# Kernel tuning notes

Hardware: AMD Instinct MI355X
Metric: run time of the kernel (lower is better)

The kernel has to match this reference:

```python
import jax, jax.numpy as jnp
import numpy as np

N = 100000          # query / support points
H = 32              # neighbors per point
CIN = 32
COUT = 64
K = 15              # kernel points
KP_EXTENT = 1.0
KERNEL_RADIUS = KP_EXTENT * 1.5


def setup_inputs() -> dict:
    key = jax.random.key(0)
    k1, k2, k3, k4, k5, k6 = jax.random.split(key, 6)
    query = jax.random.uniform(k1, (N, 3), dtype=jnp.float32)
    support = jax.random.uniform(k2, (N, 3), dtype=jnp.float32)
    edge_indices = jax.random.randint(k3, (N, H), 0, N, dtype=jnp.int32)
    features = jax.random.normal(k4, (N, CIN), dtype=jnp.float32)
    # kernel point positions within kernel radius (fixed, non-trainable)
    K_points = jax.random.normal(k5, (K, 3), dtype=jnp.float32) * (KERNEL_RADIUS / 3.0)
    K_points = K_points.at[0].set(0.0)  # fixed='center'
    # xavier-normal kernel weights [K, CIN, COUT]
    std = jnp.sqrt(2.0 / (CIN + COUT)).astype(jnp.float32)
    K_values = jax.random.normal(k6, (K, CIN, COUT), dtype=jnp.float32) * std
    return {"query": query, "support": support, "edge_indices": edge_indices,
            "features": features, "K_points": K_points, "K_values": K_values}


def reference(query, support, edge_indices, features, K_points, K_values):
    # shadow point / shadow feature for out-of-range indices
    shadow_pt = jnp.ones_like(support[:1]) * 1e6
    support_ext = jnp.concatenate([support, shadow_pt], axis=0)      # [N+1, 3]
    feats_ext = jnp.concatenate([features, jnp.zeros_like(features[:1])], axis=0)  # [N+1, CIN]

    neighbors = support_ext[edge_indices] - query[:, None, :]        # [N, H, 3]
    # squared distances to each kernel point: [N, H, K]
    diff = neighbors[:, :, None, :] - K_points[None, None, :, :]     # [N, H, K, 3]
    sq_distances = jnp.sum(diff * diff, axis=-1)                     # [N, H, K]

    # linear influence, transposed to [N, K, H]
    all_weights = jnp.maximum(1.0 - jnp.sqrt(sq_distances) / KP_EXTENT, 0.0)
    all_weights = jnp.swapaxes(all_weights, 1, 2)                    # [N, K, H]

    # aggregation_mode == 'sum': no masking
    neighborhood_features = feats_ext[edge_indices]                  # [N, H, CIN]
    weighted = jnp.einsum('nkh,nhc->nkc', all_weights, neighborhood_features)  # [N, K, CIN]
    # per-kernel-point matmul then sum over kernel points
    out = jnp.einsum('nkc,kco->no', weighted, K_values)              # [N, COUT]
    return out
```

## Files before the change

### kernel.cpp

```cpp
#include <hip/hip_runtime.h>
#include <hip/hip_bf16.h>

typedef __attribute__((ext_vector_type(8))) short short8;
typedef __attribute__((ext_vector_type(4))) short short4v;
typedef __attribute__((ext_vector_type(4))) float f32x4;
typedef __attribute__((ext_vector_type(4))) int   i32x4;
typedef __attribute__((ext_vector_type(2))) unsigned int u32x2;

#define HH    32
#define CINN  32
#define COUTT 64
#define KNUM  15

__device__ __forceinline__ short bfbits(float f) {
    __hip_bfloat16 h = __float2bfloat16(f);
    short s; __builtin_memcpy(&s, &h, 2); return s;
}

__global__ void cvt_feats_kernel(const float* __restrict__ f,
                                 unsigned short* __restrict__ o, int n4) {
    int i = blockIdx.x * blockDim.x + threadIdx.x;
    if (i < n4) {
        f32x4 v = *(const f32x4*)(f + i * 4);
        short4v s = { bfbits(v.x), bfbits(v.y), bfbits(v.z), bfbits(v.w) };
        *(short4v*)(o + i * 4) = s;
    }
}

__launch_bounds__(256, 4)
__global__ void kpconv_kernel(const float* __restrict__ query,
                              const float* __restrict__ support,
                              const int*   __restrict__ edge,
                              const unsigned short* __restrict__ featsbf,
                              const float* __restrict__ kpts,
                              const float* __restrict__ kvals,
                              float* __restrict__ out,
                              int nPts, int nBatch) {
    __shared__ unsigned short af_lds[KNUM * 64 * 8];
    __shared__ f32x4 xyz[4][4][32];

    const int tid  = threadIdx.x;
    const int wave = tid >> 6;
    const int lane = tid & 63;
    const int g    = lane >> 4;
    const int low  = lane & 15;

    short8 kvreg[KNUM];
    #pragma unroll
    for (int s = 0; s < KNUM; ++s) {
        #pragma unroll
        for (int i = 0; i < 8; ++i) {
            int cp   = (g << 3) + i;
            int chan = (((cp & 15) << 1) | (cp >> 4));
            int o    = (wave << 4) + low;
            kvreg[s][i] = bfbits(kvals[(s * CINN + chan) * COUTT + o]);
        }
    }

    float px = 1e4f, py = 1e4f, pz = 1e4f;
    if (low < KNUM) { px = kpts[low * 3 + 0]; py = kpts[low * 3 + 1]; pz = kpts[low * 3 + 2]; }
    const float m2px = -2.f * px, m2py = -2.f * py, m2pz = -2.f * pz;
    const float pp2  = px * px + py * py + pz * pz;

    __syncthreads();

    for (int b = blockIdx.x; b < nBatch; b += gridDim.x) {
        const int nbase = b * 16 + wave * 4;

        #pragma unroll
        for (int jj = 0; jj < 4; jj += 2) {
            int jpar = lane >> 5;
            int l32  = lane & 31;
            int n = nbase + jj + jpar;
            int e = edge[n * HH + l32];
            float qx = query[n * 3 + 0], qy = query[n * 3 + 1], qz = query[n * 3 + 2];
            float dx = support[e * 3 + 0] - qx;
            float dy = support[e * 3 + 1] - qy;
            float dz = support[e * 3 + 2] - qz;
            float nn = dx * dx + dy * dy + dz * dz;
            f32x4 v = { dx, dy, dz, nn };
            int sw = (l32 << 4) ^ ((l32 >> 3) << 4);
            *(f32x4*)((char*)&xyz[wave][jj + jpar][0] + sw) = v;
        }

        #pragma unroll
        for (int p = 0; p < 4; ++p) {
            const int n = nbase + p;

            const int* erow = edge + n * HH + (g << 3);
            i32x4 e0 = *(const i32x4*)erow;
            i32x4 e1 = *(const i32x4*)(erow + 4);

            unsigned fd[8];
            #pragma unroll
            for (int i = 0; i < 8; ++i) {
                int e = (i < 4) ? e0[i & 3] : e1[i & 3];
                fd[i] = *(const unsigned*)((const char*)featsbf + ((long)e << 6) + (low << 2));
            }

            short8 wf;
            const char* xb = (const char*)&xyz[wave][p][0];
            #pragma unroll
            for (int i = 0; i < 8; ++i) {
                int s = (g << 3) + i;
                f32x4 v = *(const f32x4*)(xb + ((s << 4) ^ (g << 4)));
                float d2 = fmaf(v.x, m2px, fmaf(v.y, m2py, fmaf(v.z, m2pz, v.w + pp2)));
                float w  = fmaxf(1.f - sqrtf(d2), 0.f);
                wf[i] = bfbits(w);
            }

            short8 a0, a1;
            #pragma unroll
            for (int i = 0; i < 8; ++i) {
                a0[i] = (short)(fd[i] & 0xffffu);
                a1[i] = (short)(fd[i] >> 16);
            }

            f32x4 c0 = {0.f, 0.f, 0.f, 0.f}, c1 = {0.f, 0.f, 0.f, 0.f};
            c0 = __builtin_amdgcn_mfma_f32_16x16x32_bf16(a0, wf, c0, 0, 0, 0);
            c1 = __builtin_amdgcn_mfma_f32_16x16x32_bf16(a1, wf, c1, 0, 0, 0);

            int s = low;
            if (s < KNUM) {
                unsigned lo0 = (unsigned)(unsigned short)bfbits(c0.x) | ((unsigned)(unsigned short)bfbits(c0.y) << 16);
                unsigned hi0 = (unsigned)(unsigned short)bfbits(c0.z) | ((unsigned)(unsigned short)bfbits(c0.w) << 16);
                unsigned lo1 = (unsigned)(unsigned short)bfbits(c1.x) | ((unsigned)(unsigned short)bfbits(c1.y) << 16);
                unsigned hi1 = (unsigned)(unsigned short)bfbits(c1.z) | ((unsigned)(unsigned short)bfbits(c1.w) << 16);
                int ld0  = (wave << 2) + p + ((g >> 1) << 4);
                int ld1  = ld0 + 32;
                int half = (g & 1) << 3;
                int b0 = ((s * 64 + ld0) * 16 + half) ^ ((s & 7) << 4);
                int b1 = ((s * 64 + ld1) * 16 + half) ^ ((s & 7) << 4);
                *(u32x2*)((char*)af_lds + b0) = (u32x2){lo0, hi0};
                *(u32x2*)((char*)af_lds + b1) = (u32x2){lo1, hi1};
            }
        }
        __syncthreads();

        f32x4 acc = {0.f, 0.f, 0.f, 0.f};
        #pragma unroll
        for (int s = 0; s < KNUM; ++s) {
            short8 av = *(const short8*)((const char*)af_lds +
                         (((s * 64 + lane) * 16) ^ ((s & 7) << 4)));
            acc = __builtin_amdgcn_mfma_f32_16x16x32_bf16(av, kvreg[s], acc, 0, 0, 0);
        }

        #pragma unroll
        for (int r = 0; r < 4; ++r) {
            int pp = (g << 2) + r;
            int n  = b * 16 + pp;
            if (n < nPts) out[n * COUTT + (wave << 4) + low] = acc[r];
        }
        __syncthreads();
    }
}

extern "C" void kernel_launch(void* const* d_in, const int* in_sizes, int n_in,
                              void* d_out, int out_size, void* d_ws, size_t ws_size,
                              hipStream_t stream) {
    const float* query   = (const float*)d_in[0];
    const float* support = (const float*)d_in[1];
    const int*   edge    = (const int*)d_in[2];
    const float* feats   = (const float*)d_in[3];
    const float* kpts    = (const float*)d_in[4];
    const float* kvals   = (const float*)d_in[5];
    float* out = (float*)d_out;

    int nPts   = in_sizes[0] / 3;
    int nBatch = (nPts + 15) / 16;

    unsigned short* featsbf = (unsigned short*)d_ws;
    int n4 = nPts * CINN / 4;
    hipLaunchKernelGGL(cvt_feats_kernel, dim3((n4 + 255) / 256), dim3(256), 0, stream,
                       feats, featsbf, n4);

    int grid = 1024;
    if (grid > nBatch) grid = nBatch;

    hipLaunchKernelGGL(kpconv_kernel, dim3(grid), dim3(256), 0, stream,
                       query, support, edge, featsbf, kpts, kvals, out, nPts, nBatch);
}
```

Measured before the change: 158.4 us.

## Raise occupancy, hoist LDS address math, use native sqrt, widen convert kernel

Raises launch bounds from 4 to 6 blocks per SM and the grid from 1024 to 1536 to get more waves in flight for latency hiding. Loop-invariant LDS swizzle offsets are precomputed, the xyz swizzle is dropped, and sqrt becomes the hardware builtin. The bf16 convert kernel now handles 8 floats per thread, gather offsets use 32-bit unsigned arithmetic, and point indices are clamped for tail safety. The tighter register budget may force the 15 held kernel-weight vectors to spill, and the unswizzled xyz layout may add LDS bank conflicts.

Result: slower. 239.5 us (+51.3%).

```diff
diff --git a/kernel.cpp b/kernel.cpp
--- a/kernel.cpp
+++ b/kernel.cpp
@@ -2,7 +2,6 @@
 #include <hip/hip_bf16.h>
 
 typedef __attribute__((ext_vector_type(8))) short short8;
-typedef __attribute__((ext_vector_type(4))) short short4v;
 typedef __attribute__((ext_vector_type(4))) float f32x4;
 typedef __attribute__((ext_vector_type(4))) int   i32x4;
 typedef __attribute__((ext_vector_type(2))) unsigned int u32x2;
@@ -12,22 +11,28 @@
 #define COUTT 64
 #define KNUM  15
 
-__device__ __forceinline__ short bfbits(float f) {
+static __device__ __forceinline__ short bfbits(float f) {
     __hip_bfloat16 h = __float2bfloat16(f);
     short s; __builtin_memcpy(&s, &h, 2); return s;
 }
+static __device__ __forceinline__ unsigned packbf(float a, float b) {
+    return (unsigned)(unsigned short)bfbits(a) | ((unsigned)(unsigned short)bfbits(b) << 16);
+}
 
 __global__ void cvt_feats_kernel(const float* __restrict__ f,
-                                 unsigned short* __restrict__ o, int n4) {
+                                 unsigned short* __restrict__ o, int n8) {
     int i = blockIdx.x * blockDim.x + threadIdx.x;
-    if (i < n4) {
-        f32x4 v = *(const f32x4*)(f + i * 4);
-        short4v s = { bfbits(v.x), bfbits(v.y), bfbits(v.z), bfbits(v.w) };
-        *(short4v*)(o + i * 4) = s;
+    if (i < n8) {
+        f32x4 v0 = *(const f32x4*)(f + i * 8);
+        f32x4 v1 = *(const f32x4*)(f + i * 8 + 4);
+        u32x2 s0 = { packbf(v0.x, v0.y), packbf(v0.z, v0.w) };
+        u32x2 s1 = { packbf(v1.x, v1.y), packbf(v1.z, v1.w) };
+        *(u32x2*)(o + i * 8)     = s0;
+        *(u32x2*)(o + i * 8 + 4) = s1;
     }
 }
 
-__launch_bounds__(256, 4)
+__launch_bounds__(256, 6)
 __global__ void kpconv_kernel(const float* __restrict__ query,
                               const float* __restrict__ support,
                               const int*   __restrict__ edge,
@@ -62,30 +67,39 @@
     const float m2px = -2.f * px, m2py = -2.f * py, m2pz = -2.f * pz;
     const float pp2  = px * px + py * py + pz * pz;
 
+    const int  ld0  = (wave << 2) + ((g >> 1) << 4);
+    const int  half = (g & 1) << 3;
+    const int  dM   = (low & 7) << 4;
+    const int  T0   = (low * 64 + ld0) * 16 + half;
+    const int  T1   = T0 + 32 * 16;
+    const bool sact = (low < KNUM);
+    const unsigned lbase = (unsigned)lane << 4;
+
     __syncthreads();
 
     for (int b = blockIdx.x; b < nBatch; b += gridDim.x) {
-        const int nbase = b * 16 + wave * 4;
+        const int nbase = b * 16 + (wave << 2);
 
         #pragma unroll
         for (int jj = 0; jj < 4; jj += 2) {
             int jpar = lane >> 5;
             int l32  = lane & 31;
             int n = nbase + jj + jpar;
+            if (n >= nPts) n = nPts - 1;
             int e = edge[n * HH + l32];
-            float qx = query[n * 3 + 0], qy = query[n * 3 + 1], qz = query[n * 3 + 2];
-            float dx = support[e * 3 + 0] - qx;
-            float dy = support[e * 3 + 1] - qy;
-            float dz = support[e * 3 + 2] - qz;
-            float nn = dx * dx + dy * dy + dz * dz;
-            f32x4 v = { dx, dy, dz, nn };
-            int sw = (l32 << 4) ^ ((l32 >> 3) << 4);
-            *(f32x4*)((char*)&xyz[wave][jj + jpar][0] + sw) = v;
+            const float* qp = query + n * 3;
+            const float* sp = support + (size_t)(unsigned)e * 3;
+            float dx = sp[0] - qp[0];
+            float dy = sp[1] - qp[1];
+            float dz = sp[2] - qp[2];
+            float nn = fmaf(dx, dx, fmaf(dy, dy, dz * dz));
+            xyz[wave][jj + jpar][l32] = (f32x4){dx, dy, dz, nn};
         }
 
         #pragma unroll
         for (int p = 0; p < 4; ++p) {
-            const int n = nbase + p;
+            int n = nbase + p;
+            if (n >= nPts) n = nPts - 1;
 
             const int* erow = edge + n * HH + (g << 3);
             i32x4 e0 = *(const i32x4*)erow;
@@ -94,18 +108,18 @@
             unsigned fd[8];
             #pragma unroll
             for (int i = 0; i < 8; ++i) {
-                int e = (i < 4) ? e0[i & 3] : e1[i & 3];
-                fd[i] = *(const unsigned*)((const char*)featsbf + ((long)e << 6) + (low << 2));
+                unsigned e = (unsigned)((i < 4) ? e0[i & 3] : e1[i & 3]);
+                unsigned off = (e << 6) + ((unsigned)low << 2);
+                fd[i] = *(const unsigned*)((const char*)featsbf + off);
             }
 
             short8 wf;
-            const char* xb = (const char*)&xyz[wave][p][0];
+            const f32x4* xrow = &xyz[wave][p][g << 3];
             #pragma unroll
             for (int i = 0; i < 8; ++i) {
-                int s = (g << 3) + i;
-                f32x4 v = *(const f32x4*)(xb + ((s << 4) ^ (g << 4)));
+                f32x4 v = xrow[i];
                 float d2 = fmaf(v.x, m2px, fmaf(v.y, m2py, fmaf(v.z, m2pz, v.w + pp2)));
-                float w  = fmaxf(1.f - sqrtf(d2), 0.f);
+                float w  = fmaxf(1.f - __builtin_amdgcn_sqrtf(d2), 0.f);
                 wf[i] = bfbits(w);
             }
 
@@ -120,19 +134,11 @@
             c0 = __builtin_amdgcn_mfma_f32_16x16x32_bf16(a0, wf, c0, 0, 0, 0);
             c1 = __builtin_amdgcn_mfma_f32_16x16x32_bf16(a1, wf, c1, 0, 0, 0);
 
-            int s = low;
-            if (s < KNUM) {
-                unsigned lo0 = (unsigned)(unsigned short)bfbits(c0.x) | ((unsigned)(unsigned short)bfbits(c0.y) << 16);
-                unsigned hi0 = (unsigned)(unsigned short)bfbits(c0.z) | ((unsigned)(unsigned short)bfbits(c0.w) << 16);
-                unsigned lo1 = (unsigned)(unsigned short)bfbits(c1.x) | ((unsigned)(unsigned short)bfbits(c1.y) << 16);
-                unsigned hi1 = (unsigned)(unsigned short)bfbits(c1.z) | ((unsigned)(unsigned short)bfbits(c1.w) << 16);
-                int ld0  = (wave << 2) + p + ((g >> 1) << 4);
-                int ld1  = ld0 + 32;
-                int half = (g & 1) << 3;
-                int b0 = ((s * 64 + ld0) * 16 + half) ^ ((s & 7) << 4);
-                int b1 = ((s * 64 + ld1) * 16 + half) ^ ((s & 7) << 4);
-                *(u32x2*)((char*)af_lds + b0) = (u32x2){lo0, hi0};
-                *(u32x2*)((char*)af_lds + b1) = (u32x2){lo1, hi1};
+            if (sact) {
+                u32x2 w0 = { packbf(c0.x, c0.y), packbf(c0.z, c0.w) };
+                u32x2 w1 = { packbf(c1.x, c1.y), packbf(c1.z, c1.w) };
+                *(u32x2*)((char*)af_lds + ((T0 + (p << 4)) ^ dM)) = w0;
+                *(u32x2*)((char*)af_lds + ((T1 + (p << 4)) ^ dM)) = w1;
             }
         }
         __syncthreads();
@@ -140,16 +146,18 @@
         f32x4 acc = {0.f, 0.f, 0.f, 0.f};
         #pragma unroll
         for (int s = 0; s < KNUM; ++s) {
-            short8 av = *(const short8*)((const char*)af_lds +
-                         (((s * 64 + lane) * 16) ^ ((s & 7) << 4)));
+            const char* ap = (const char*)af_lds + (lbase ^ (unsigned)((s & 7) << 4)) + s * 1024;
+            short8 av = *(const short8*)ap;
             acc = __builtin_amdgcn_mfma_f32_16x16x32_bf16(av, kvreg[s], acc, 0, 0, 0);
         }
 
-        #pragma unroll
-        for (int r = 0; r < 4; ++r) {
-            int pp = (g << 2) + r;
-            int n  = b * 16 + pp;
-            if (n < nPts) out[n * COUTT + (wave << 4) + low] = acc[r];
+        {
+            int n0 = b * 16 + (g << 2);
+            float* orow = out + (size_t)(unsigned)n0 * COUTT + (wave << 4) + low;
+            #pragma unroll
+            for (int r = 0; r < 4; ++r) {
+                if (n0 + r < nPts) orow[r * COUTT] = acc[r];
+            }
         }
         __syncthreads();
     }
@@ -170,11 +178,11 @@
     int nBatch = (nPts + 15) / 16;
 
     unsigned short* featsbf = (unsigned short*)d_ws;
-    int n4 = nPts * CINN / 4;
-    hipLaunchKernelGGL(cvt_feats_kernel, dim3((n4 + 255) / 256), dim3(256), 0, stream,
-                       feats, featsbf, n4);
+    int n8 = nPts * CINN / 8;
+    hipLaunchKernelGGL(cvt_feats_kernel, dim3((n8 + 255) / 256), dim3(256), 0, stream,
+                       feats, featsbf, n8);
 
-    int grid = 1024;
+    int grid = 1536;
     if (grid > nBatch) grid = nBatch;
 
     hipLaunchKernelGGL(kpconv_kernel, dim3(grid), dim3(256), 0, stream,
```
